# Optimization experiments

Measured on AMD Instinct MI355X. Metric: run time of the kernel, lower is better.

The kernel has to match this reference:

```python
import jax, jax.numpy as jnp
import numpy as np

BETA = 0.25
EPS = 1e-12  # torch F.normalize eps


def _l2_normalize(x, axis):
    n = jnp.linalg.norm(x, axis=axis, keepdims=True)
    return x / jnp.maximum(n, EPS)


def setup_inputs() -> dict:
    key = jax.random.key(0)
    k1, k2 = jax.random.split(key)
    z = jax.random.normal(k1, (16, 256, 64, 64), dtype=jnp.float32)
    K = 1024
    embedding = jax.random.uniform(k2, (K, 256), dtype=jnp.float32,
                                   minval=-1.0 / K, maxval=1.0 / K)
    return {"z": z, "embedding": embedding}


def reference(z, embedding):
    # Faithful to torch source: normalize over the LAST axis of [B,C,H,W] (the W axis)
    zn = _l2_normalize(z, axis=-1)
    zp = jnp.transpose(zn, (0, 2, 3, 1))            # [B,H,W,C]
    B, H, W, C = zp.shape
    zf = zp.reshape(-1, C)                           # [N, C], N = B*H*W
    wn = _l2_normalize(embedding, axis=-1)           # normalized codebook for distances
    # d[n,k] = ||zf_n||^2 + ||wn_k||^2 - 2 zf_n . wn_k
    d = (jnp.sum(zf * zf, axis=1, keepdims=True)
         + jnp.sum(wn * wn, axis=1)
         - 2.0 * jnp.einsum('nc,kc->nk', zf, wn))
    idx = jnp.argmin(d, axis=1)                      # [N] int
    # gather uses the UN-normalized embedding (as in torch source)
    z_q = embedding[idx].reshape(B, H, W, C)
    # training-mode commitment loss + straight-through estimator
    loss = (BETA * jnp.mean((jax.lax.stop_gradient(z_q) - zp) ** 2)
            + jnp.mean((z_q - jax.lax.stop_gradient(zp)) ** 2))
    z_q = zp + jax.lax.stop_gradient(z_q - zp)
    z_q = jnp.transpose(z_q, (0, 3, 1, 2))           # back to [B,C,H,W]
    return z_q, idx, loss
```

## Files before the change

kernel.cpp:

```cpp
#include <hip/hip_runtime.h>

#define NN 65536
#define KK 1024
#define TFLAG_FIX 2098u

typedef __bf16 bf16x8 __attribute__((ext_vector_type(8)));
typedef float f32x16 __attribute__((ext_vector_type(16)));

__device__ __forceinline__ unsigned short f2bf(float x){
  unsigned u = __float_as_uint(x);
  u += 0x7FFFu + ((u >> 16) & 1u);
  return (unsigned short)(u >> 16);
}
__device__ __forceinline__ float bf2f(unsigned short h){
  return __uint_as_float(((unsigned)h) << 16);
}
__device__ __forceinline__ void dma16(const uint4* g, uint4* l){
  __builtin_amdgcn_global_load_lds(
      (const __attribute__((address_space(1))) void*)g,
      (__attribute__((address_space(3))) void*)l, 16, 0, 0);
}
__device__ __forceinline__ unsigned long long shfl_xor_u64(unsigned long long v, int m){
  unsigned lo = (unsigned)__shfl_xor((int)(unsigned)v, m, 64);
  unsigned hi = (unsigned)__shfl_xor((int)(unsigned)(v >> 32), m, 64);
  return ((unsigned long long)hi << 32) | lo;
}
union U4S8 { uint4 v; unsigned short u[8]; };


__global__ __launch_bounds__(64) void kern_prep(const float* __restrict__ emb,
    float* __restrict__ wnT, uint4* __restrict__ wnh4,
    float* __restrict__ wnn, float* __restrict__ wnn4)
{
  const int k = blockIdx.x, t = threadIdx.x;
  float4 v = ((const float4*)emb)[k*64 + t];
  float ss = fmaf(v.x, v.x, fmaf(v.y, v.y, fmaf(v.z, v.z, v.w * v.w)));
  #pragma unroll
  for (int m = 32; m > 0; m >>= 1) ss += __shfl_xor(ss, m, 64);
  float d = fmaxf(sqrtf(ss), 1e-12f);
  float w0 = v.x / d, w1 = v.y / d, w2 = v.z / d, w3 = v.w / d;
  wnT[(size_t)(4*t+0)*1024 + k] = w0;
  wnT[(size_t)(4*t+1)*1024 + k] = w1;
  wnT[(size_t)(4*t+2)*1024 + k] = w2;
  wnT[(size_t)(4*t+3)*1024 + k] = w3;
  unsigned short* base = (unsigned short*)wnh4;
  size_t o = ((size_t)(k >> 5) * 1024 + (size_t)(t >> 1) * 32 + (k & 31)) * 8 + (t & 1) * 4;
  base[o+0] = f2bf(w0); base[o+1] = f2bf(w1); base[o+2] = f2bf(w2); base[o+3] = f2bf(w3);
  float s2 = fmaf(w0, w0, fmaf(w1, w1, fmaf(w2, w2, w3 * w3)));
  #pragma unroll
  for (int m = 32; m > 0; m >>= 1) s2 += __shfl_xor(s2, m, 64);
  if (t == 0){ wnn[k] = s2; wnn4[k] = 4.0f - s2; }
}

__global__ __launch_bounds__(256) void kern_znorm(const float* __restrict__ z,
    uint4* __restrict__ zfh4, uint4* __restrict__ zfl4)
{
  __shared__ float tile[64][65];
  __shared__ float sinv[64];
  const int t = threadIdx.x;
  const int ct = blockIdx.x & 3;
  const int bh = blockIdx.x >> 2;
  const int c0 = ct * 64, q0 = ct * 8;
  const int cl = t >> 2, q = t & 3;
  const float4* zr = (const float4*)(z + ((size_t)(bh >> 6) * 256 + c0 + cl) * 4096
                                       + (size_t)(bh & 63) * 64);
  #pragma unroll
  for (int i = 0; i < 4; i++){
    float4 v = zr[q + 4*i];
    int w = (q + 4*i) * 4;
    tile[cl][w] = v.x; tile[cl][w+1] = v.y; tile[cl][w+2] = v.z; tile[cl][w+3] = v.w;
  }
  __syncthreads();
  if (t < 64){
    float ss = 0.f;
    #pragma unroll
    for (int w = 0; w < 64; w++){ float x = tile[t][w]; ss = fmaf(x, x, ss); }
    sinv[t] = 1.0f / fmaxf(sqrtf(ss), 1e-12f);
  }
  __syncthreads();
  #pragma unroll
  for (int j = 0; j < 2; j++){
    int p = t + 256 * j;
    int tI = p >> 8, rem = p & 255;
    int qq = rem >> 5, colI = rem & 31;
    int w = tI * 32 + colI;
    U4S8 hh, ll;
    #pragma unroll
    for (int e = 0; e < 8; e++){
      int c = qq * 8 + e;
      float v = tile[c][w] * sinv[c];
      hh.u[e] = f2bf(v);
      ll.u[e] = f2bf(v - bf2f(hh.u[e]));
    }
    size_t o = (size_t)(bh * 2 + tI) * 1024 + (size_t)(q0 + qq) * 32 + colI;
    zfh4[o] = hh.v;
    zfl4[o] = ll.v;
  }
}

__global__ __launch_bounds__(256, 2) void kern_gemm(
    const uint4* __restrict__ zA, const uint4* __restrict__ wB,
    const float* __restrict__ wnn4, uint2* __restrict__ pairs)
{
  __shared__ uint4 sB[2][1024];
  const int t = threadIdx.x;
  const int wv = t >> 6;
  const int lane = t & 63;
  const int col = lane & 31;
  const int half = lane >> 5;
  const int hb = blockIdx.x & 1;
  const int cb = hb * 512;
  const int rowBase = (blockIdx.x >> 1) * 256 + wv * 64;
  const int T0 = rowBase >> 5;

  bf16x8 a0[16], a1[16];
  {
    const uint4* r0 = zA + (size_t)T0 * 1024;
    const uint4* r1 = zA + (size_t)(T0 + 1) * 1024;
    const uint4* g0 = wB + (size_t)(cb >> 5) * 1024;
    dma16(g0 + (wv*4+0)*64 + lane, &sB[0][(wv*4+0)*64 + lane]);
    dma16(g0 + (wv*4+1)*64 + lane, &sB[0][(wv*4+1)*64 + lane]);
    dma16(g0 + (wv*4+2)*64 + lane, &sB[0][(wv*4+2)*64 + lane]);
    dma16(g0 + (wv*4+3)*64 + lane, &sB[0][(wv*4+3)*64 + lane]);
    #pragma unroll
    for (int s = 0; s < 16; s++){
      a0[s] = __builtin_bit_cast(bf16x8, r0[(2*s + half)*32 + col]);
      a1[s] = __builtin_bit_cast(bf16x8, r1[(2*s + half)*32 + col]);
    }
  }
  unsigned b1k[2][16], b2k[2][16];
  #pragma unroll
  for (int r = 0; r < 16; r++){
    b1k[0][r] = 0u; b1k[1][r] = 0u; b2k[0][r] = 0u; b2k[1][r] = 0u;
  }
  const int kinvBase = 1023 - cb - col;
  __syncthreads();

  for (int kt = 0; kt < 16; kt++){
    if (kt < 15){
      const uint4* gn = wB + (size_t)((cb >> 5) + kt + 1) * 1024;
      uint4* ld = &sB[(kt + 1) & 1][0];
      dma16(gn + (wv*4+0)*64 + lane, ld + (wv*4+0)*64 + lane);
      dma16(gn + (wv*4+1)*64 + lane, ld + (wv*4+1)*64 + lane);
      dma16(gn + (wv*4+2)*64 + lane, ld + (wv*4+2)*64 + lane);
      dma16(gn + (wv*4+3)*64 + lane, ld + (wv*4+3)*64 + lane);
    }
    const float c4k = wnn4[cb + kt*32 + col];
    const uint4* bp = &sB[kt & 1][half * 32 + col];
    f32x16 acc0, acc1;
    #pragma unroll
    for (int i = 0; i < 16; i++){ acc0[i] = 0.0f; acc1[i] = 0.0f; }
    #pragma unroll
    for (int s = 0; s < 16; s++){
      bf16x8 bs = __builtin_bit_cast(bf16x8, bp[s * 64]);
      acc0 = __builtin_amdgcn_mfma_f32_32x32x16_bf16(a0[s], bs, acc0, 0, 0, 0);
      acc1 = __builtin_amdgcn_mfma_f32_32x32x16_bf16(a1[s], bs, acc1, 0, 0, 0);
    }
    const unsigned kinv = (unsigned)(kinvBase - kt * 32);
    #pragma unroll
    for (int r = 0; r < 16; r++){
      float s0 = fmaf(2.0f, acc0[r], c4k);
      unsigned u0 = ((unsigned)(s0 * 524288.0f) << 10) | kinv;
      b2k[0][r] = max(b2k[0][r], min(b1k[0][r], u0));
      b1k[0][r] = max(b1k[0][r], u0);
      float s1 = fmaf(2.0f, acc1[r], c4k);
      unsigned u1 = ((unsigned)(s1 * 524288.0f) << 10) | kinv;
      b2k[1][r] = max(b2k[1][r], min(b1k[1][r], u1));
      b1k[1][r] = max(b1k[1][r], u1);
    }
    __syncthreads();
  }
  #pragma unroll
  for (int m = 1; m < 32; m <<= 1){
    #pragma unroll
    for (int ti = 0; ti < 2; ti++){
      #pragma unroll
      for (int r = 0; r < 16; r++){
        unsigned o1 = (unsigned)__shfl_xor((int)b1k[ti][r], m, 64);
        unsigned o2 = (unsigned)__shfl_xor((int)b2k[ti][r], m, 64);
        b2k[ti][r] = max(max(b2k[ti][r], o2), min(b1k[ti][r], o1));
        b1k[ti][r] = max(b1k[ti][r], o1);
      }
    }
  }
  if (col == 0){
    #pragma unroll
    for (int ti = 0; ti < 2; ti++){
      #pragma unroll
      for (int r = 0; r < 16; r++){
        int rowD = (r & 3) + 8 * (r >> 2) + 4 * half;
        int n = rowBase + ti * 32 + rowD;
        pairs[(size_t)n * 2 + hb] = make_uint2(b1k[ti][r], b2k[ti][r]);
      }
    }
  }
}

__global__ __launch_bounds__(256) void kern_merge(
    const uint2* __restrict__ pairs, int* __restrict__ idx_i, float* __restrict__ idx_f,
    int* __restrict__ flag_list, unsigned int* __restrict__ flag_count)
{
  const int n = blockIdx.x * 256 + threadIdx.x;
  uint2 p0 = pairs[(size_t)n * 2];
  uint2 p1 = pairs[(size_t)n * 2 + 1];
  unsigned B1 = max(p0.x, p1.x);
  unsigned B2 = max(max(p0.y, p1.y), min(p0.x, p1.x));
  int idx = 1023 - (int)(B1 & 1023u);
  idx_i[n] = idx;
  idx_f[n] = (float)idx;
  bool f = ((B1 >> 10) - (B2 >> 10)) < TFLAG_FIX;
  unsigned long long m = __ballot(f);
  if (m){
    int lane = threadIdx.x & 63;
    int leader = __ffsll((unsigned long long)m) - 1;
    unsigned base = 0;
    if (lane == leader) base = atomicAdd(flag_count, (unsigned)__popcll(m));
    base = (unsigned)__shfl((int)base, leader, 64);
    if (f){
      int off = __popcll(m & ((1ull << lane) - 1ull));
      flag_list[base + off] = n;
    }
  }
}

struct RescueSM {
  float sz[16][256];
  unsigned long long sred[4][16];
  int srow[16];
};
struct GatherSM {
  float zq[64][65];
  int sidx[64];
  float swsum[4];
};

__global__ __launch_bounds__(256) void kern_fused(
    const float* __restrict__ z, const float* __restrict__ emb,
    const int* __restrict__ idx_i, float* __restrict__ out,
    float* __restrict__ loss_acc,
    const uint4* __restrict__ zfh4, const uint4* __restrict__ zfl4,
    const float* __restrict__ wnT, const float* __restrict__ wnn,
    const int* __restrict__ flag_list, const unsigned int* __restrict__ flag_count,
    unsigned long long* __restrict__ keys)
{
  __shared__ union { RescueSM r; GatherSM g; } sm;
  const int t = threadIdx.x;

  if (blockIdx.x < 1024){
    const int lane = t & 63, wvi = t >> 6;
    const int cnt = (int)*flag_count;
    const int hb = blockIdx.x & 1;
    const int bb = blockIdx.x >> 1;
    if (bb * 16 >= cnt) return;
    const int k0 = hb * 512 + t * 2;
    const float wq0 = wnn[k0+0], wq1 = wnn[k0+1];
    const float2* wt2 = (const float2*)wnT;
    const size_t ko2 = (size_t)(k0 >> 1);

    for (int base = bb * 16; base < cnt; base += 512 * 16){
      const int nr = min(16, cnt - base);
      __syncthreads();
      if (t < 16) sm.r.srow[t] = flag_list[base + min(t, nr - 1)];
      __syncthreads();
      #pragma unroll
      for (int j = 0; j < 2; j++){
        int p = t + j * 256;
        int r = p >> 5, q = p & 31;
        int n = sm.r.srow[r];
        size_t o = (size_t)(n >> 5) * 1024 + (size_t)q * 32 + (n & 31);
        U4S8 h, l; h.v = zfh4[o]; l.v = zfl4[o];
        #pragma unroll
        for (int e = 0; e < 8; e++) sm.r.sz[r][q*8+e] = bf2f(h.u[e]) + bf2f(l.u[e]);
      }
      __syncthreads();

      float acc[2][16];
      #pragma unroll
      for (int j = 0; j < 2; j++)
        #pragma unroll
        for (int r = 0; r < 16; r++) acc[j][r] = 0.0f;
      for (int c4 = 0; c4 < 64; c4++){
        float2 cv0 = wt2[(size_t)(4*c4+0)*512 + ko2];
        float2 cv1 = wt2[(size_t)(4*c4+1)*512 + ko2];
        float2 cv2 = wt2[(size_t)(4*c4+2)*512 + ko2];
        float2 cv3 = wt2[(size_t)(4*c4+3)*512 + ko2];
        #pragma unroll
        for (int r = 0; r < 16; r++){
          float4 s = ((const float4*)sm.r.sz[r])[c4];
          acc[0][r] = fmaf(s.x, cv0.x, acc[0][r]);
          acc[0][r] = fmaf(s.y, cv1.x, acc[0][r]);
          acc[0][r] = fmaf(s.z, cv2.x, acc[0][r]);
          acc[0][r] = fmaf(s.w, cv3.x, acc[0][r]);
          acc[1][r] = fmaf(s.x, cv0.y, acc[1][r]);
          acc[1][r] = fmaf(s.y, cv1.y, acc[1][r]);
          acc[1][r] = fmaf(s.z, cv2.y, acc[1][r]);
          acc[1][r] = fmaf(s.w, cv3.y, acc[1][r]);
        }
      }
      #pragma unroll
      for (int r = 0; r < 16; r++){
        float s0 = fmaf(-2.0f, acc[0][r], wq0);
        float s1 = fmaf(-2.0f, acc[1][r], wq1);
        float bv = s0; int bi = k0;
        if (s1 < bv){ bv = s1; bi = k0 + 1; }
        unsigned u = __float_as_uint(bv);
        u = (u & 0x80000000u) ? ~u : (u | 0x80000000u);
        unsigned long long key = ((unsigned long long)u << 10) | (unsigned)bi;
        #pragma unroll
        for (int m = 1; m < 64; m <<= 1){
          unsigned long long o = shfl_xor_u64(key, m);
          if (o < key) key = o;
        }
        if (lane == 0) sm.r.sred[wvi][r] = key;
      }
      __syncthreads();
      if (t < nr){
        unsigned long long ka = sm.r.sred[0][t] < sm.r.sred[1][t] ? sm.r.sred[0][t] : sm.r.sred[1][t];
        unsigned long long kb = sm.r.sred[2][t] < sm.r.sred[3][t] ? sm.r.sred[2][t] : sm.r.sred[3][t];
        unsigned long long kf = ka < kb ? ka : kb;
        keys[(size_t)sm.r.srow[t] * 2 + hb] = kf;
      }
    }
    return;
  }

  const int gb = blockIdx.x - 1024;
  const int ct = gb & 3;
  const int bh = gb >> 2;
  const int c0 = ct * 64;
  if (t < 64) sm.g.sidx[t] = idx_i[bh*64 + t];

  const int r = t >> 2, w0 = (t & 3) * 16;
  const float4* zr = (const float4*)(z + ((size_t)(bh >> 6) * 256 + c0 + r) * 4096
                                       + (size_t)(bh & 63) * 64 + w0);
  float4 tz0 = zr[0], tz1 = zr[1], tz2 = zr[2], tz3 = zr[3];
  __syncthreads();

  {
    const int ch4 = (t & 15) * 4, wrow = t >> 4;
    #pragma unroll
    for (int it = 0; it < 4; it++){
      int w = wrow + 16*it;
      float4 qv = *(const float4*)(emb + (size_t)sm.g.sidx[w] * 256 + c0 + ch4);
      sm.g.zq[ch4+0][w] = qv.x; sm.g.zq[ch4+1][w] = qv.y;
      sm.g.zq[ch4+2][w] = qv.z; sm.g.zq[ch4+3][w] = qv.w;
    }
  }
  float ss = 0.f;
  ss = fmaf(tz0.x, tz0.x, ss); ss = fmaf(tz0.y, tz0.y, ss);
  ss = fmaf(tz0.z, tz0.z, ss); ss = fmaf(tz0.w, tz0.w, ss);
  ss = fmaf(tz1.x, tz1.x, ss); ss = fmaf(tz1.y, tz1.y, ss);
  ss = fmaf(tz1.z, tz1.z, ss); ss = fmaf(tz1.w, tz1.w, ss);
  ss = fmaf(tz2.x, tz2.x, ss); ss = fmaf(tz2.y, tz2.y, ss);
  ss = fmaf(tz2.z, tz2.z, ss); ss = fmaf(tz2.w, tz2.w, ss);
  ss = fmaf(tz3.x, tz3.x, ss); ss = fmaf(tz3.y, tz3.y, ss);
  ss = fmaf(tz3.z, tz3.z, ss); ss = fmaf(tz3.w, tz3.w, ss);
  ss += __shfl_xor(ss, 1, 64);
  ss += __shfl_xor(ss, 2, 64);
  const float inv = 1.0f / fmaxf(sqrtf(ss), 1e-12f);
  __syncthreads();

  float lsum = 0.f;
  float* op = out + ((size_t)(bh >> 6) * 256 + c0 + r) * 4096
                  + (size_t)(bh & 63) * 64 + w0;
  #pragma unroll
  for (int i = 0; i < 4; i++){
    float4 tzv = (i == 0) ? tz0 : (i == 1) ? tz1 : (i == 2) ? tz2 : tz3;
    int w = w0 + 4*i;
    float q0 = sm.g.zq[r][w+0], q1 = sm.g.zq[r][w+1];
    float q2 = sm.g.zq[r][w+2], q3 = sm.g.zq[r][w+3];
    float d0 = q0 - tzv.x * inv;
    float d1 = q1 - tzv.y * inv;
    float d2 = q2 - tzv.z * inv;
    float d3 = q3 - tzv.w * inv;
    lsum = fmaf(d0, d0, lsum); lsum = fmaf(d1, d1, lsum);
    lsum = fmaf(d2, d2, lsum); lsum = fmaf(d3, d3, lsum);
    ((float4*)op)[i] = make_float4(q0, q1, q2, q3);
  }
  #pragma unroll
  for (int m = 32; m > 0; m >>= 1) lsum += __shfl_down(lsum, m, 64);
  if ((t & 63) == 0) sm.g.swsum[t >> 6] = lsum;
  __syncthreads();
  if (t == 0) atomicAdd(loss_acc, sm.g.swsum[0] + sm.g.swsum[1] + sm.g.swsum[2] + sm.g.swsum[3]);
}

__global__ __launch_bounds__(256) void kern_patch(
    const uint4* __restrict__ zfh4, const uint4* __restrict__ zfl4,
    const float* __restrict__ emb, const unsigned long long* __restrict__ keys,
    const int* __restrict__ flag_list, const unsigned int* __restrict__ flag_count,
    const int* __restrict__ idx_i, float* __restrict__ out_idx,
    float* __restrict__ out, float* __restrict__ loss_acc)
{
  const int cnt = (int)*flag_count;
  const int wvi = threadIdx.x >> 6, lane = threadIdx.x & 63;
  float dsum = 0.f;
  for (int i = blockIdx.x * 4 + wvi; i < cnt; i += gridDim.x * 4){
    const int n = flag_list[i];
    unsigned long long ka = keys[(size_t)n * 2];
    unsigned long long kb = keys[(size_t)n * 2 + 1];
    unsigned long long kf = ka < kb ? ka : kb;
    const int fi = (int)(kf & 1023ull);
    const int old = idx_i[n];
    if (fi == old) continue;
    if (lane == 0) out_idx[n] = (float)fi;
    if (lane < 32){
      size_t o = (size_t)(n >> 5) * 1024 + (size_t)lane * 32 + (n & 31);
      U4S8 h, l; h.v = zfh4[o]; l.v = zfl4[o];
      const float4* eo4 = (const float4*)(emb + (size_t)old * 256 + lane * 8);
      const float4* en4 = (const float4*)(emb + (size_t)fi  * 256 + lane * 8);
      float4 eo0 = eo4[0], eo1 = eo4[1];
      float4 en0 = en4[0], en1 = en4[1];
      float zp[8];
      #pragma unroll
      for (int e = 0; e < 8; e++) zp[e] = bf2f(h.u[e]) + bf2f(l.u[e]);
      float dn, do_;
      dn = en0.x - zp[0]; do_ = eo0.x - zp[0]; dsum += dn*dn - do_*do_;
      dn = en0.y - zp[1]; do_ = eo0.y - zp[1]; dsum += dn*dn - do_*do_;
      dn = en0.z - zp[2]; do_ = eo0.z - zp[2]; dsum += dn*dn - do_*do_;
      dn = en0.w - zp[3]; do_ = eo0.w - zp[3]; dsum += dn*dn - do_*do_;
      dn = en1.x - zp[4]; do_ = eo1.x - zp[4]; dsum += dn*dn - do_*do_;
      dn = en1.y - zp[5]; do_ = eo1.y - zp[5]; dsum += dn*dn - do_*do_;
      dn = en1.z - zp[6]; do_ = eo1.z - zp[6]; dsum += dn*dn - do_*do_;
      dn = en1.w - zp[7]; do_ = eo1.w - zp[7]; dsum += dn*dn - do_*do_;
      float* ob = out + ((size_t)(n >> 12) * 256 + lane * 8) * 4096 + (n & 4095);
      ob[0*4096] = en0.x; ob[1*4096] = en0.y; ob[2*4096] = en0.z; ob[3*4096] = en0.w;
      ob[4*4096] = en1.x; ob[5*4096] = en1.y; ob[6*4096] = en1.z; ob[7*4096] = en1.w;
    }
  }
  #pragma unroll
  for (int m = 1; m < 32; m <<= 1) dsum += __shfl_xor(dsum, m, 64);
  if (lane == 0 && dsum != 0.f) atomicAdd(loss_acc, dsum);
}

__global__ void kern_final(const float* __restrict__ loss_acc, float* __restrict__ out_loss){
  if (threadIdx.x == 0 && blockIdx.x == 0)
    out_loss[0] = 1.25f * loss_acc[0] * (1.0f / 16777216.0f);
}

extern "C" void kernel_launch(void* const* d_in, const int* in_sizes, int n_in,
                              void* d_out, int out_size, void* d_ws, size_t ws_size,
                              hipStream_t stream)
{
  const float* z   = (const float*)d_in[0];
  const float* emb = (const float*)d_in[1];
  char* ws = (char*)d_ws;
  unsigned int* flag_count = (unsigned int*)(ws + 0);
  float* loss_acc          = (float*)(ws + 8);
  float* wnn               = (float*)(ws + 1024);
  float* wnn4              = (float*)(ws + 8192);
  float* wnT               = (float*)(ws + 16384);
  uint4* wnh4              = (uint4*)(ws + 1064960);
  int* idx_i               = (int*)(ws + 1589248);
  int* flag_list           = (int*)(ws + 1851392);
  uint2* pairs             = (uint2*)(ws + 2113536);
  unsigned long long* keys = (unsigned long long*)(ws + 2113536);
  uint4* zfh4              = (uint4*)(ws + 3162112);
  uint4* zfl4              = (uint4*)(ws + 36716544);
  float* out_zq   = (float*)d_out;
  float* out_idx  = (float*)d_out + 16777216;
  float* out_loss = (float*)d_out + 16842752;

  hipMemsetAsync(ws, 0, 16, stream);
  kern_prep<<<KK, 64, 0, stream>>>(emb, wnT, wnh4, wnn, wnn4);
  kern_znorm<<<4096, 256, 0, stream>>>(z, zfh4, zfl4);
  kern_gemm<<<512, 256, 0, stream>>>(zfh4, wnh4, wnn4, pairs);
  kern_merge<<<256, 256, 0, stream>>>(pairs, idx_i, out_idx, flag_list, flag_count);
  kern_fused<<<5120, 256, 0, stream>>>(z, emb, idx_i, out_zq, loss_acc,
                                       zfh4, zfl4, wnT, wnn, flag_list, flag_count,
                                       keys);
  kern_patch<<<128, 256, 0, stream>>>(zfh4, zfl4, emb, keys, flag_list, flag_count,
                                      idx_i, out_idx, out_zq, loss_acc);
  kern_final<<<1, 64, 0, stream>>>(loss_acc, out_loss);
}
```

Baseline: 272.3 us.

## Restructure fp32 rescue pass to per-thread rows with atomicMin key reduction

The fp32 rescue of flagged rows now processes 32 rows per block. Each thread owns one row and 32 codebook entries, read from a row-major normalized codebook instead of the transposed one. The 64-lane shuffle argmin reduction and the shared-memory cross-wave merge are replaced by a per-thread running minimum and a global 64-bit atomicMin into a single key per row, which kern_merge initializes. This removes shuffle and sync overhead but adds global atomics and uncoalesced per-thread codebook reads. The keys buffer is relocated to overlap the bf16 codebook region, which is reused after the GEMM.

After: 315.7 us. 15.9% more time.

```diff
diff --git a/kernel.cpp b/kernel.cpp
--- a/kernel.cpp
+++ b/kernel.cpp
@@ -20,16 +20,11 @@
       (const __attribute__((address_space(1))) void*)g,
       (__attribute__((address_space(3))) void*)l, 16, 0, 0);
 }
-__device__ __forceinline__ unsigned long long shfl_xor_u64(unsigned long long v, int m){
-  unsigned lo = (unsigned)__shfl_xor((int)(unsigned)v, m, 64);
-  unsigned hi = (unsigned)__shfl_xor((int)(unsigned)(v >> 32), m, 64);
-  return ((unsigned long long)hi << 32) | lo;
-}
 union U4S8 { uint4 v; unsigned short u[8]; };
 
 
 __global__ __launch_bounds__(64) void kern_prep(const float* __restrict__ emb,
-    float* __restrict__ wnT, uint4* __restrict__ wnh4,
+    float* __restrict__ wn, uint4* __restrict__ wnh4,
     float* __restrict__ wnn, float* __restrict__ wnn4)
 {
   const int k = blockIdx.x, t = threadIdx.x;
@@ -39,10 +34,7 @@
   for (int m = 32; m > 0; m >>= 1) ss += __shfl_xor(ss, m, 64);
   float d = fmaxf(sqrtf(ss), 1e-12f);
   float w0 = v.x / d, w1 = v.y / d, w2 = v.z / d, w3 = v.w / d;
-  wnT[(size_t)(4*t+0)*1024 + k] = w0;
-  wnT[(size_t)(4*t+1)*1024 + k] = w1;
-  wnT[(size_t)(4*t+2)*1024 + k] = w2;
-  wnT[(size_t)(4*t+3)*1024 + k] = w3;
+  ((float4*)wn)[k*64 + t] = make_float4(w0, w1, w2, w3);
   unsigned short* base = (unsigned short*)wnh4;
   size_t o = ((size_t)(k >> 5) * 1024 + (size_t)(t >> 1) * 32 + (k & 31)) * 8 + (t & 1) * 4;
   base[o+0] = f2bf(w0); base[o+1] = f2bf(w1); base[o+2] = f2bf(w2); base[o+3] = f2bf(w3);
@@ -198,7 +190,8 @@
 
 __global__ __launch_bounds__(256) void kern_merge(
     const uint2* __restrict__ pairs, int* __restrict__ idx_i, float* __restrict__ idx_f,
-    int* __restrict__ flag_list, unsigned int* __restrict__ flag_count)
+    int* __restrict__ flag_list, unsigned int* __restrict__ flag_count,
+    unsigned long long* __restrict__ keys)
 {
   const int n = blockIdx.x * 256 + threadIdx.x;
   uint2 p0 = pairs[(size_t)n * 2];
@@ -219,14 +212,14 @@
     if (f){
       int off = __popcll(m & ((1ull << lane) - 1ull));
       flag_list[base + off] = n;
+      keys[n] = ~0ull;
     }
   }
 }
 
 struct RescueSM {
-  float sz[16][256];
-  unsigned long long sred[4][16];
-  int srow[16];
+  float sz[32][260];
+  int srow[32];
 };
 struct GatherSM {
   float zq[64][65];
@@ -239,7 +232,7 @@
     const int* __restrict__ idx_i, float* __restrict__ out,
     float* __restrict__ loss_acc,
     const uint4* __restrict__ zfh4, const uint4* __restrict__ zfl4,
-    const float* __restrict__ wnT, const float* __restrict__ wnn,
+    const float* __restrict__ wn, const float* __restrict__ wnn,
     const int* __restrict__ flag_list, const unsigned int* __restrict__ flag_count,
     unsigned long long* __restrict__ keys)
 {
@@ -249,21 +242,19 @@
   if (blockIdx.x < 1024){
     const int lane = t & 63, wvi = t >> 6;
     const int cnt = (int)*flag_count;
-    const int hb = blockIdx.x & 1;
-    const int bb = blockIdx.x >> 1;
-    if (bb * 16 >= cnt) return;
-    const int k0 = hb * 512 + t * 2;
-    const float wq0 = wnn[k0+0], wq1 = wnn[k0+1];
-    const float2* wt2 = (const float2*)wnT;
-    const size_t ko2 = (size_t)(k0 >> 1);
-
-    for (int base = bb * 16; base < cnt; base += 512 * 16){
-      const int nr = min(16, cnt - base);
+    const int g0 = blockIdx.x >> 2;
+    const int slice = (blockIdx.x & 3) * 4 + wvi;
+    const int kbase = slice * 64 + (lane >> 5) * 32;
+    const int row = lane & 31;
+
+    for (int gg = g0; gg * 32 < cnt; gg += 256){
+      const int base = gg * 32;
+      const int nr = min(32, cnt - base);
       __syncthreads();
-      if (t < 16) sm.r.srow[t] = flag_list[base + min(t, nr - 1)];
+      if (t < 32) sm.r.srow[t] = flag_list[base + min(t, nr - 1)];
       __syncthreads();
       #pragma unroll
-      for (int j = 0; j < 2; j++){
+      for (int j = 0; j < 4; j++){
         int p = t + j * 256;
         int r = p >> 5, q = p & 31;
         int n = sm.r.srow[r];
@@ -274,52 +265,40 @@
       }
       __syncthreads();
 
-      float acc[2][16];
-      #pragma unroll
-      for (int j = 0; j < 2; j++)
+      float acc[32];
+      #pragma unroll
+      for (int k = 0; k < 32; k++) acc[k] = 0.0f;
+      const float* sr = sm.r.sz[row];
+      for (int ch = 0; ch < 16; ch++){
+        const float4* zp4 = (const float4*)(sr + ch * 16);
+        float4 z0 = zp4[0], z1 = zp4[1], z2 = zp4[2], z3 = zp4[3];
+        const float* wb = wn + (size_t)kbase * 256 + ch * 16;
         #pragma unroll
-        for (int r = 0; r < 16; r++) acc[j][r] = 0.0f;
-      for (int c4 = 0; c4 < 64; c4++){
-        float2 cv0 = wt2[(size_t)(4*c4+0)*512 + ko2];
-        float2 cv1 = wt2[(size_t)(4*c4+1)*512 + ko2];
-        float2 cv2 = wt2[(size_t)(4*c4+2)*512 + ko2];
-        float2 cv3 = wt2[(size_t)(4*c4+3)*512 + ko2];
-        #pragma unroll
-        for (int r = 0; r < 16; r++){
-          float4 s = ((const float4*)sm.r.sz[r])[c4];
-          acc[0][r] = fmaf(s.x, cv0.x, acc[0][r]);
-          acc[0][r] = fmaf(s.y, cv1.x, acc[0][r]);
-          acc[0][r] = fmaf(s.z, cv2.x, acc[0][r]);
-          acc[0][r] = fmaf(s.w, cv3.x, acc[0][r]);
-          acc[1][r] = fmaf(s.x, cv0.y, acc[1][r]);
-          acc[1][r] = fmaf(s.y, cv1.y, acc[1][r]);
-          acc[1][r] = fmaf(s.z, cv2.y, acc[1][r]);
-          acc[1][r] = fmaf(s.w, cv3.y, acc[1][r]);
+        for (int k = 0; k < 32; k++){
+          const float4* wp = (const float4*)(wb + (size_t)k * 256);
+          float4 w0 = wp[0], w1 = wp[1], w2 = wp[2], w3 = wp[3];
+          float a = acc[k];
+          a = fmaf(z0.x, w0.x, a); a = fmaf(z0.y, w0.y, a);
+          a = fmaf(z0.z, w0.z, a); a = fmaf(z0.w, w0.w, a);
+          a = fmaf(z1.x, w1.x, a); a = fmaf(z1.y, w1.y, a);
+          a = fmaf(z1.z, w1.z, a); a = fmaf(z1.w, w1.w, a);
+          a = fmaf(z2.x, w2.x, a); a = fmaf(z2.y, w2.y, a);
+          a = fmaf(z2.z, w2.z, a); a = fmaf(z2.w, w2.w, a);
+          a = fmaf(z3.x, w3.x, a); a = fmaf(z3.y, w3.y, a);
+          a = fmaf(z3.z, w3.z, a); a = fmaf(z3.w, w3.w, a);
+          acc[k] = a;
         }
       }
-      #pragma unroll
-      for (int r = 0; r < 16; r++){
-        float s0 = fmaf(-2.0f, acc[0][r], wq0);
-        float s1 = fmaf(-2.0f, acc[1][r], wq1);
-        float bv = s0; int bi = k0;
-        if (s1 < bv){ bv = s1; bi = k0 + 1; }
-        unsigned u = __float_as_uint(bv);
+      unsigned long long best = ~0ull;
+      #pragma unroll
+      for (int k = 0; k < 32; k++){
+        float s = fmaf(-2.0f, acc[k], wnn[kbase + k]);
+        unsigned u = __float_as_uint(s);
         u = (u & 0x80000000u) ? ~u : (u | 0x80000000u);
-        unsigned long long key = ((unsigned long long)u << 10) | (unsigned)bi;
-        #pragma unroll
-        for (int m = 1; m < 64; m <<= 1){
-          unsigned long long o = shfl_xor_u64(key, m);
-          if (o < key) key = o;
-        }
-        if (lane == 0) sm.r.sred[wvi][r] = key;
+        unsigned long long key = ((unsigned long long)u << 10) | (unsigned)(kbase + k);
+        best = key < best ? key : best;
       }
-      __syncthreads();
-      if (t < nr){
-        unsigned long long ka = sm.r.sred[0][t] < sm.r.sred[1][t] ? sm.r.sred[0][t] : sm.r.sred[1][t];
-        unsigned long long kb = sm.r.sred[2][t] < sm.r.sred[3][t] ? sm.r.sred[2][t] : sm.r.sred[3][t];
-        unsigned long long kf = ka < kb ? ka : kb;
-        keys[(size_t)sm.r.srow[t] * 2 + hb] = kf;
-      }
+      atomicMin(&keys[(size_t)sm.r.srow[row]], best);
     }
     return;
   }
@@ -396,9 +375,7 @@
   float dsum = 0.f;
   for (int i = blockIdx.x * 4 + wvi; i < cnt; i += gridDim.x * 4){
     const int n = flag_list[i];
-    unsigned long long ka = keys[(size_t)n * 2];
-    unsigned long long kb = keys[(size_t)n * 2 + 1];
-    unsigned long long kf = ka < kb ? ka : kb;
+    unsigned long long kf = keys[n];
     const int fi = (int)(kf & 1023ull);
     const int old = idx_i[n];
     if (fi == old) continue;
@@ -448,12 +425,12 @@
   float* loss_acc          = (float*)(ws + 8);
   float* wnn               = (float*)(ws + 1024);
   float* wnn4              = (float*)(ws + 8192);
-  float* wnT               = (float*)(ws + 16384);
+  float* wn                = (float*)(ws + 16384);
   uint4* wnh4              = (uint4*)(ws + 1064960);
+  unsigned long long* keys = (unsigned long long*)(ws + 1064960);
   int* idx_i               = (int*)(ws + 1589248);
   int* flag_list           = (int*)(ws + 1851392);
   uint2* pairs             = (uint2*)(ws + 2113536);
-  unsigned long long* keys = (unsigned long long*)(ws + 2113536);
   uint4* zfh4              = (uint4*)(ws + 3162112);
   uint4* zfl4              = (uint4*)(ws + 36716544);
   float* out_zq   = (float*)d_out;
@@ -461,12 +438,13 @@
   float* out_loss = (float*)d_out + 16842752;
 
   hipMemsetAsync(ws, 0, 16, stream);
-  kern_prep<<<KK, 64, 0, stream>>>(emb, wnT, wnh4, wnn, wnn4);
+  kern_prep<<<KK, 64, 0, stream>>>(emb, wn, wnh4, wnn, wnn4);
   kern_znorm<<<4096, 256, 0, stream>>>(z, zfh4, zfl4);
   kern_gemm<<<512, 256, 0, stream>>>(zfh4, wnh4, wnn4, pairs);
-  kern_merge<<<256, 256, 0, stream>>>(pairs, idx_i, out_idx, flag_list, flag_count);
+  kern_merge<<<256, 256, 0, stream>>>(pairs, idx_i, out_idx, flag_list, flag_count,
+                                      keys);
   kern_fused<<<5120, 256, 0, stream>>>(z, emb, idx_i, out_zq, loss_acc,
-                                       zfh4, zfl4, wnT, wnn, flag_list, flag_count,
+                                       zfh4, zfl4, wn, wnn, flag_list, flag_count,
                                        keys);
   kern_patch<<<128, 256, 0, stream>>>(zfh4, zfl4, emb, keys, flag_list, flag_count,
                                       idx_i, out_idx, out_zq, loss_acc);
```
